# Performance work log

Measured on AMD Instinct MI355X. Metric: run time of the kernel, lower is better.

## Reference

```python
import jax, jax.numpy as jnp
import numpy as np

HIDDEN_DIM = 64


def setup_inputs() -> dict:
    key = jax.random.key(0)
    k1, k2, k3, k4, k5 = jax.random.split(key, 5)
    B, C, H, W = 4, HIDDEN_DIM, 80, 80
    query = jax.random.normal(k1, (B, C, H, W), dtype=jnp.float32)
    keys = jax.random.normal(k2, (B, C, H, W), dtype=jnp.float32)
    values = jax.random.normal(k3, (B, C, H, W), dtype=jnp.float32)
    # 1x1 conv == per-pixel linear: weight [C_out, C_in], bias [C_out]
    fan_in = C  # kernel_size=1 -> fan_in = C*1*1
    bound = 1.0 / np.sqrt(fan_in)
    Wq = jax.random.uniform(k4, (C, C), dtype=jnp.float32, minval=-bound, maxval=bound)
    bq = jax.random.uniform(k5, (C,), dtype=jnp.float32, minval=-bound, maxval=bound)
    return {"query": query, "keys": keys, "values": values, "Wq": Wq, "bq": bq}


def reference(query, keys, values, Wq, bq):
    B, C, H, W = query.shape
    scale = C ** (-0.5)
    # 1x1 conv projection of query
    qp = jnp.einsum('bchw,dc->bdhw', query, Wq) + bq[None, :, None, None]
    q = qp.reshape(B, C, H * W).transpose(0, 2, 1)       # [B, N, C]
    k = keys.reshape(B, C, H * W)                        # [B, C, N]
    attn = jax.nn.softmax(jnp.einsum('bnc,bcm->bnm', q, k) * scale, axis=-1)  # [B, N, N]
    v = values.reshape(B, C, H * W).transpose(0, 2, 1)   # [B, N, C]
    context = jnp.einsum('bnm,bmc->bnc', attn, v)        # [B, N, C]
    return context.transpose(0, 2, 1).reshape(B, C, H, W)
```

## Files before the change

kernel.cpp:

```cpp
#include <hip/hip_runtime.h>
#include <hip/hip_bf16.h>


#define NPIX 6400
#define SZ 1638400
#define SHIFT2 11.541560327111707f

typedef float f32x4 __attribute__((ext_vector_type(4)));
typedef short bf16x8 __attribute__((ext_vector_type(8)));

#if defined(__has_builtin)
#if __has_builtin(__builtin_amdgcn_sched_barrier)
#define SCHED_FENCE() __builtin_amdgcn_sched_barrier(0)
#endif
#if __has_builtin(__builtin_amdgcn_exp2f)
#define EXP2(x) __builtin_amdgcn_exp2f(x)
#endif
#endif
#ifndef SCHED_FENCE
#define SCHED_FENCE()
#endif
#ifndef EXP2
#define EXP2(x) exp2f(x)
#endif

__device__ __forceinline__ void split2(float x, short& h, short& l) {
  unsigned xb = __float_as_uint(x);
  h = (short)(xb >> 16);
  float r = x - __uint_as_float(xb & 0xffff0000u);
  l = (short)(__float_as_uint(r) >> 16);
}

__device__ __forceinline__ short rne_bf16(float x) {
  unsigned u = __float_as_uint(x);
  return (short)((u + 0x7fffu + ((u >> 16) & 1u)) >> 16);
}

__device__ __forceinline__ unsigned pk2(float a, float b) {
  __hip_bfloat162 t = __float22bfloat162_rn(make_float2(a, b));
  unsigned r;
  __builtin_memcpy(&r, &t, 4);
  return r;
}

__global__ __launch_bounds__(256, 2) void prep(
    const float* __restrict__ query, const float* __restrict__ keys,
    const float* __restrict__ values, const float* __restrict__ Wq,
    const float* __restrict__ bq, short* __restrict__ ws)
{
  const int tid = threadIdx.x;
  const int w = tid >> 6;
  const int lane = tid & 63, l16 = lane & 15, qq = lane >> 4;
  short* Qh = ws;          short* Ql = ws + SZ;
  short* Kh = ws + 2 * SZ; short* Kl = ws + 3 * SZ;
  short* Vh = ws + 4 * SZ;
  const int x = blockIdx.x;

  __shared__ float T[64 * 65];

  if (x < 400) {
    const int b = x / 100, t64 = x % 100;
    const int m0 = t64 * 64;
    const float* kb = keys + (size_t)b * 64 * NPIX;
    {
      const int ch = tid >> 2, ml = (tid & 3) * 4;
      const float* src = kb + (size_t)ch * NPIX + m0 + ml;
      #pragma unroll
      for (int u = 0; u < 4; ++u)
        *(float4*)&T[ch * 65 + ml + 16 * u] = *(const float4*)(src + 16 * u);
    }
    __syncthreads();
    const int mi = t64 * 4 + w;
    #pragma unroll
    for (int c0 = 0; c0 < 2; ++c0) {
      float t[8];
      #pragma unroll
      for (int j = 0; j < 8; ++j)
        t[j] = T[(32 * c0 + 8 * qq + j) * 65 + 16 * w + l16];
      bf16x8 h8, l8;
      #pragma unroll
      for (int j = 0; j < 8; ++j) { short h, l; split2(t[j], h, l); h8[j] = h; l8[j] = l; }
      const int off = ((b * 400 + mi) * 2 + c0) * 512 + lane * 8;
      *(bf16x8*)(Kh + off) = h8;
      *(bf16x8*)(Kl + off) = l8;
    }
  } else if (x < 800) {
    const int y = x - 400;
    const int b = y / 100, t64 = y % 100;
    const int r0 = t64 * 64;
    const float* qb = query + (size_t)b * 64 * NPIX;
    {
      const int ch = tid >> 2, ml = (tid & 3) * 4;
      const float* src = qb + (size_t)ch * NPIX + r0 + ml;
      #pragma unroll
      for (int u = 0; u < 4; ++u)
        *(float4*)&T[ch * 65 + ml + 16 * u] = *(const float4*)(src + 16 * u);
    }
    __syncthreads();
    const int mi = t64 * 4 + w;

    float acc[2][8];
    #pragma unroll
    for (int c0 = 0; c0 < 2; ++c0)
      #pragma unroll
      for (int j = 0; j < 8; ++j) acc[c0][j] = 0.f;

    for (int cin4 = 0; cin4 < 64; cin4 += 4) {
      float xv[4];
      #pragma unroll
      for (int u = 0; u < 4; ++u)
        xv[u] = T[(cin4 + u) * 65 + 16 * w + l16];
      #pragma unroll
      for (int c0 = 0; c0 < 2; ++c0)
        #pragma unroll
        for (int j = 0; j < 8; ++j) {
          const float4 wv = *(const float4*)&Wq[(32 * c0 + 8 * qq + j) * 64 + cin4];
          acc[c0][j] += wv.x * xv[0] + wv.y * xv[1] + wv.z * xv[2] + wv.w * xv[3];
        }
    }
    #pragma unroll
    for (int c0 = 0; c0 < 2; ++c0) {
      bf16x8 h8, l8;
      #pragma unroll
      for (int j = 0; j < 8; ++j) {
        float v = (acc[c0][j] + bq[32 * c0 + 8 * qq + j]) * 0.18033688011112042f;
        short h, l; split2(v, h, l);
        h8[j] = h; l8[j] = l;
      }
      const int off = ((b * 400 + mi) * 2 + c0) * 512 + lane * 8;
      *(bf16x8*)(Qh + off) = h8;
      *(bf16x8*)(Ql + off) = l8;
    }
  } else {
    const int gw = (x - 800) * 4 + w;
    const int b = gw / 200, rest = gw % 200;
    const int i = rest / 2, half = rest % 2;
    const float* vb = values + (size_t)b * 64 * NPIX;
    #pragma unroll
    for (int cc = 0; cc < 2; ++cc) {
      const int ct = 2 * half + cc;
      #pragma unroll
      for (int mh = 0; mh < 2; ++mh) {
        const float* vp = vb + (size_t)(16 * ct + l16) * NPIX + 64 * i + 32 * mh + 8 * qq;
        const float4 a  = *(const float4*)vp;
        const float4 b4 = *(const float4*)(vp + 4);
        const float t[8] = {a.x, a.y, a.z, a.w, b4.x, b4.y, b4.z, b4.w};
        bf16x8 h8;
        #pragma unroll
        for (int j = 0; j < 8; ++j) h8[j] = rne_bf16(t[j]);
        const int off = (((b * 100 + i) * 8) + ct * 2 + mh) * 512 + lane * 8;
        *(bf16x8*)(Vh + off) = h8;
      }
    }
  }
}

__global__ __launch_bounds__(512, 1) void attn_main(
    const short* __restrict__ ws, float* __restrict__ out)
{
  const int tid  = threadIdx.x;
  const int w    = tid >> 6;
  const int lane = tid & 63;
  const int l16  = lane & 15, qq = lane >> 4;
  const int x = blockIdx.x;
  const int b      = x & 3;
  const int rowjob = x >> 2;
  const int rb     = rowjob * 64;

  const short* Qh = ws;
  const short* Kh = ws + 2 * SZ;
  const short* Vh = ws + 4 * SZ;
  float* ob = out + (size_t)b * 64 * NPIX;

  __shared__ char smem[43008];
  short* P   = ((short*)smem) + (w << 11);
  short* QL  = ((short*)smem) + 16384;
  float* OC  = (float*)smem;
  float* LST = (float*)(smem + 40960);

  bf16x8 qfh[4][2];
  {
    const short* qp = Qh + (size_t)((b * 400 + rowjob * 4) * 2) * 512 + lane * 8;
    #pragma unroll
    for (int s = 0; s < 4; ++s)
      #pragma unroll
      for (int c0 = 0; c0 < 2; ++c0) {
        qfh[s][c0] = *(const bf16x8*)(qp + (s * 2 + c0) * 512);
        *(bf16x8*)(QL + ((s * 2 + c0) * 64 + lane) * 8) =
            *(const bf16x8*)(qp + SZ + (s * 2 + c0) * 512);
      }
  }
  __syncthreads();

  f32x4 zero4 = {0.f, 0.f, 0.f, 0.f};
  f32x4 oacc[4][4];
  f32x4 lacc[4];
  #pragma unroll
  for (int ct = 0; ct < 4; ++ct)
    #pragma unroll
    for (int s = 0; s < 4; ++s) oacc[ct][s] = zero4;
  #pragma unroll
  for (int s = 0; s < 4; ++s) lacc[s] = zero4;

  bf16x8 onesA;
  #pragma unroll
  for (int j = 0; j < 8; ++j) onesA[j] = (short)0x3F80;

  bf16x8 kfh[2][2], kfl[2][2];
  bf16x8 vfh[4];

  auto loadK = [&](int i2) {
    const short* kp = Kh + (size_t)((b * 400 + 2 * i2) * 2) * 512 + lane * 8;
    #pragma unroll
    for (int mt = 0; mt < 2; ++mt)
      #pragma unroll
      for (int c0 = 0; c0 < 2; ++c0) {
        kfh[mt][c0] = *(const bf16x8*)(kp + (mt * 2 + c0) * 512);
        kfl[mt][c0] = *(const bf16x8*)(kp + SZ + (mt * 2 + c0) * 512);
      }
  };
  auto loadV = [&](int i2) {
    const short* vp = Vh + (size_t)((b * 100 + (i2 >> 1)) * 8) * 512 + lane * 8;
    #pragma unroll
    for (int ct = 0; ct < 4; ++ct)
      vfh[ct] = *(const bf16x8*)(vp + (ct * 2 + (i2 & 1)) * 512);
  };

  const int i0 = w * 25;
  loadK(i0);
  loadV(i0);

  for (int it = 0; it < 25; ++it) {
    const int i2 = i0 + it;
    const int inext = (it == 24) ? i0 : i2 + 1;

    f32x4 a0[4], a1[4];
    #pragma unroll
    for (int s = 0; s < 4; ++s) {
      f32x4 t0 = zero4, t1 = zero4;
      #pragma unroll
      for (int c0 = 0; c0 < 2; ++c0) {
        const bf16x8 ql = *(const bf16x8*)(QL + ((s * 2 + c0) * 64 + lane) * 8);
        t0 = __builtin_amdgcn_mfma_f32_16x16x32_bf16(kfh[0][c0], qfh[s][c0], t0, 0, 0, 0);
        t0 = __builtin_amdgcn_mfma_f32_16x16x32_bf16(kfh[0][c0], ql,         t0, 0, 0, 0);
        t0 = __builtin_amdgcn_mfma_f32_16x16x32_bf16(kfl[0][c0], qfh[s][c0], t0, 0, 0, 0);
        t1 = __builtin_amdgcn_mfma_f32_16x16x32_bf16(kfh[1][c0], qfh[s][c0], t1, 0, 0, 0);
        t1 = __builtin_amdgcn_mfma_f32_16x16x32_bf16(kfh[1][c0], ql,         t1, 0, 0, 0);
        t1 = __builtin_amdgcn_mfma_f32_16x16x32_bf16(kfl[1][c0], qfh[s][c0], t1, 0, 0, 0);
      }
      a0[s] = t0; a1[s] = t1;
    }

    SCHED_FENCE();
    loadK(inext);
    SCHED_FENCE();

    #pragma unroll
    for (int s = 0; s < 4; ++s) {
      float p0 = EXP2(a0[s][0] - SHIFT2), p1 = EXP2(a0[s][1] - SHIFT2);
      float p2 = EXP2(a0[s][2] - SHIFT2), p3 = EXP2(a0[s][3] - SHIFT2);
      float p4 = EXP2(a1[s][0] - SHIFT2), p5 = EXP2(a1[s][1] - SHIFT2);
      float p6 = EXP2(a1[s][2] - SHIFT2), p7 = EXP2(a1[s][3] - SHIFT2);
      union { unsigned u[2]; short4 s4; } ua, ub;
      ua.u[0] = pk2(p0, p1); ua.u[1] = pk2(p2, p3);
      ub.u[0] = pk2(p4, p5); ub.u[1] = pk2(p6, p7);
      const int gbase = (s * 4 + (qq >> 1)) * 16 + l16;
      *(short4*)(P + (gbase * 8 + 4 * (qq & 1))) = ua.s4;
      *(short4*)(P + ((gbase + 32) * 8 + 4 * (qq & 1))) = ub.s4;
    }

    bf16x8 pf[4];
    #pragma unroll
    for (int s = 0; s < 4; ++s)
      pf[s] = *(const bf16x8*)(P + (((s * 4 + qq) * 16 + l16) * 8));

    #pragma unroll
    for (int ct = 0; ct < 4; ++ct)
      #pragma unroll
      for (int s = 0; s < 4; ++s)
        oacc[ct][s] = __builtin_amdgcn_mfma_f32_16x16x32_bf16(vfh[ct], pf[s], oacc[ct][s], 0, 0, 0);
    #pragma unroll
    for (int s = 0; s < 4; ++s)
      lacc[s] = __builtin_amdgcn_mfma_f32_16x16x32_bf16(onesA, pf[s], lacc[s], 0, 0, 0);

    SCHED_FENCE();
    loadV(inext);
    SCHED_FENCE();
  }

  if (qq == 0) {
    #pragma unroll
    for (int s = 0; s < 4; ++s) LST[w * 64 + s * 16 + l16] = lacc[s][0];
  }
  __syncthreads();

  #pragma unroll
  for (int wp = 0; wp < 8; ++wp) {
    if (w == wp) {
      #pragma unroll
      for (int ct = 0; ct < 4; ++ct)
        #pragma unroll
        for (int s = 0; s < 4; ++s)
          #pragma unroll
          for (int r = 0; r < 4; ++r) {
            const int c = 16 * ct + 4 * qq + r;
            const int idx = c * 65 + 16 * s + l16;
            if (wp == 0) OC[idx] = oacc[ct][s][r];
            else         OC[idx] += oacc[ct][s][r];
          }
    }
    __syncthreads();
  }

  {
    const int r  = tid & 63;
    const int cg = tid >> 6;
    float lsum = 0.f;
    #pragma unroll
    for (int w2 = 0; w2 < 8; ++w2)
      lsum += LST[w2 * 64 + (r >> 4) * 16 + (r & 15)];
    const float inv = 1.0f / lsum;
    #pragma unroll
    for (int u = 0; u < 8; ++u) {
      const int c = cg * 8 + u;
      ob[(size_t)c * NPIX + rb + r] = OC[c * 65 + r] * inv;
    }
  }
}

extern "C" void kernel_launch(void* const* d_in, const int* in_sizes, int n_in,
                              void* d_out, int out_size, void* d_ws, size_t ws_size,
                              hipStream_t stream) {
  const float* query  = (const float*)d_in[0];
  const float* keys   = (const float*)d_in[1];
  const float* values = (const float*)d_in[2];
  const float* Wq     = (const float*)d_in[3];
  const float* bq     = (const float*)d_in[4];
  short* ws = (short*)d_ws;
  prep<<<dim3(1000), dim3(256), 0, stream>>>(query, keys, values, Wq, bq, ws);
  attn_main<<<dim3(400), dim3(512), 0, stream>>>(ws, (float*)d_out);
}
```

Before: 183.4 us.

## Software-pipeline QK^T of next tile with PV of current tile, drop sched barriers

Restructures the main attention loop into a software pipeline. Each iteration computes the score MFMAs for the next key tile while doing the P·V and row-sum MFMAs for the current tile, with a prologue and epilogue added. The intent is to overlap the exp/softmax and LDS round-trip with matrix work and to let the compiler interleave instructions freely, since the sched_barrier fences are removed. This raises register pressure because scores, loaded P fragments and K/V fragments are live at once, and correctness depends on the P buffer not being overwritten before it is read.

```diff
diff --git a/kernel.cpp b/kernel.cpp
--- a/kernel.cpp
+++ b/kernel.cpp
@@ -10,15 +10,9 @@
 typedef short bf16x8 __attribute__((ext_vector_type(8)));
 
 #if defined(__has_builtin)
-#if __has_builtin(__builtin_amdgcn_sched_barrier)
-#define SCHED_FENCE() __builtin_amdgcn_sched_barrier(0)
-#endif
 #if __has_builtin(__builtin_amdgcn_exp2f)
 #define EXP2(x) __builtin_amdgcn_exp2f(x)
 #endif
-#endif
-#ifndef SCHED_FENCE
-#define SCHED_FENCE()
 #endif
 #ifndef EXP2
 #define EXP2(x) exp2f(x)
@@ -226,15 +220,9 @@
       vfh[ct] = *(const bf16x8*)(vp + (ct * 2 + (i2 & 1)) * 512);
   };
 
-  const int i0 = w * 25;
-  loadK(i0);
-  loadV(i0);
-
-  for (int it = 0; it < 25; ++it) {
-    const int i2 = i0 + it;
-    const int inext = (it == 24) ? i0 : i2 + 1;
-
-    f32x4 a0[4], a1[4];
+  f32x4 a0[4], a1[4];
+
+  auto computeS = [&]() {
     #pragma unroll
     for (int s = 0; s < 4; ++s) {
       f32x4 t0 = zero4, t1 = zero4;
@@ -250,11 +238,9 @@
       }
       a0[s] = t0; a1[s] = t1;
     }
-
-    SCHED_FENCE();
-    loadK(inext);
-    SCHED_FENCE();
-
+  };
+
+  auto softmaxStore = [&]() {
     #pragma unroll
     for (int s = 0; s < 4; ++s) {
       float p0 = EXP2(a0[s][0] - SHIFT2), p1 = EXP2(a0[s][1] - SHIFT2);
@@ -268,11 +254,23 @@
       *(short4*)(P + (gbase * 8 + 4 * (qq & 1))) = ua.s4;
       *(short4*)(P + ((gbase + 32) * 8 + 4 * (qq & 1))) = ub.s4;
     }
-
+  };
+
+  const int i0 = w * 25;
+
+  loadK(i0);
+  loadV(i0);
+  computeS();
+  loadK(i0 + 1);
+  softmaxStore();
+
+  for (int j = 0; j < 24; ++j) {
     bf16x8 pf[4];
     #pragma unroll
     for (int s = 0; s < 4; ++s)
       pf[s] = *(const bf16x8*)(P + (((s * 4 + qq) * 16 + l16) * 8));
+
+    computeS();
 
     #pragma unroll
     for (int ct = 0; ct < 4; ++ct)
@@ -283,9 +281,24 @@
     for (int s = 0; s < 4; ++s)
       lacc[s] = __builtin_amdgcn_mfma_f32_16x16x32_bf16(onesA, pf[s], lacc[s], 0, 0, 0);
 
-    SCHED_FENCE();
-    loadV(inext);
-    SCHED_FENCE();
+    loadV(i0 + j + 1);
+    softmaxStore();
+    loadK(j + 2 <= 24 ? i0 + j + 2 : i0);
+  }
+
+  {
+    bf16x8 pf[4];
+    #pragma unroll
+    for (int s = 0; s < 4; ++s)
+      pf[s] = *(const bf16x8*)(P + (((s * 4 + qq) * 16 + l16) * 8));
+    #pragma unroll
+    for (int ct = 0; ct < 4; ++ct)
+      #pragma unroll
+      for (int s = 0; s < 4; ++s)
+        oacc[ct][s] = __builtin_amdgcn_mfma_f32_16x16x32_bf16(vfh[ct], pf[s], oacc[ct][s], 0, 0, 0);
+    #pragma unroll
+    for (int s = 0; s < 4; ++s)
+      lacc[s] = __builtin_amdgcn_mfma_f32_16x16x32_bf16(onesA, pf[s], lacc[s], 0, 0, 0);
   }
 
   if (qq == 0) {
```

Result: no change. 183.3 us (-0.1%).
